# Performance work log

Hardware: AMD Instinct MI355X
Metric: run time of the kernel (lower is better)

Reference implementation:

```python
import jax, jax.numpy as jnp
import numpy as np

H, E, DFF = 1024, 8, 4096


def setup_inputs() -> dict:
    key = jax.random.key(0)
    ks = jax.random.split(key, 7)
    s = lambda *shape: 1.0 / np.sqrt(shape[-2] if len(shape) > 1 else shape[-1])
    x = jax.random.normal(ks[0], (2, 2048, H), dtype=jnp.float32)
    Wr = jax.random.normal(ks[1], (H, E), dtype=jnp.float32) * (1.0 / np.sqrt(H))
    br = jnp.zeros((E,), dtype=jnp.float32)
    W1 = jax.random.normal(ks[2], (E, H, DFF), dtype=jnp.float32) * (1.0 / np.sqrt(H))
    b1 = jnp.zeros((E, DFF), dtype=jnp.float32)
    W2 = jax.random.normal(ks[3], (E, DFF, H), dtype=jnp.float32) * (1.0 / np.sqrt(DFF))
    b2 = jnp.zeros((E, H), dtype=jnp.float32)
    return {"x": x, "Wr": Wr, "br": br, "W1": W1, "b1": b1, "W2": W2, "b2": b2}


def reference(x, Wr, br, W1, b1, W2, b2):
    B, S, Hd = x.shape
    n_exp = W1.shape[0]
    xt = x.reshape(-1, Hd)                      # (T, H)
    logits = xt @ Wr + br                       # (T, E)
    probs = jax.nn.softmax(logits, axis=-1)
    gate = jnp.max(probs, axis=-1)              # (T,) top-1 gate value
    idx = jnp.argmax(probs, axis=-1)            # (T,) chosen expert
    # dense all-expert FFN, then one-hot combine (vectorized equivalent of per-token loop)
    h1 = jnp.maximum(jnp.einsum('th,ehf->etf', xt, W1) + b1[:, None, :], 0.0)  # (E,T,DFF)
    ye = jnp.einsum('etf,efh->eth', h1, W2) + b2[:, None, :]                   # (E,T,H)
    onehot = jax.nn.one_hot(idx, n_exp, dtype=xt.dtype)                        # (T,E)
    y = jnp.einsum('te,eth->th', onehot, ye) * gate[:, None]                   # (T,H)
    return y.reshape(B, S, Hd)
```

## Files before the change

kernel.cpp:

```cpp
#include <hip/hip_runtime.h>
#include <stdint.h>

typedef unsigned short u16;
typedef __attribute__((ext_vector_type(8))) short s16x8;
typedef __attribute__((ext_vector_type(4))) float f32x4;
typedef __attribute__((ext_vector_type(4))) unsigned uint4v;

#define NEXP 8
#define HD 1024
#define DFF 4096
#define BM 128
#define BN 128
#define BK 64

#define CT_S 136
#define TILE_U16 (BM * BK)

__device__ __forceinline__ u16 f2bf(float f) {
  union { float f; unsigned u; } c; c.f = f;
  unsigned r = c.u + 0x7fffu + ((c.u >> 16) & 1u);
  return (u16)(r >> 16);
}

__device__ __forceinline__ unsigned cvtpk(float a, float b) {
  unsigned r;
  asm("v_cvt_pk_bf16_f32 %0, %1, %2" : "=v"(r) : "v"(a), "v"(b));
  return r;
}

__device__ __forceinline__ void gload_lds16(const void* g, const void* l) {
  __builtin_amdgcn_global_load_lds(
      (const __attribute__((address_space(1))) unsigned int*)(uintptr_t)g,
      (__attribute__((address_space(3))) unsigned int*)(unsigned)(uintptr_t)l,
      16, 0, 0);
}

__global__ __launch_bounds__(64) void zero_k(int* counts) {
  if (threadIdx.x < NEXP) counts[threadIdx.x] = 0;
}

template <int K, int N>
__device__ __forceinline__ void convt_tile(const float* __restrict__ W,
    u16* __restrict__ Wt, int idx, u16* __restrict__ T) {
  const int e = idx >> 9;
  const int ti = idx & 511;
  const int k0 = (ti % (K / 128)) * 128;
  const int n0 = (ti / (K / 128)) * 64;
  const float* src = W + (size_t)e * K * N;
  u16* dst = Wt + (size_t)e * K * N;
  const int t = threadIdx.x;
  const int m = t & 15, g = t >> 4;
  const int kq = g * 8, nq = m * 4;
  f32x4 v[8];
#pragma unroll
  for (int i = 0; i < 8; ++i)
    v[i] = *(const f32x4*)(src + (size_t)(k0 + kq + i) * N + n0 + nq);
#pragma unroll
  for (int j = 0; j < 4; ++j) {
    uint4v q;
    q[0] = cvtpk(v[0][j], v[1][j]);
    q[1] = cvtpk(v[2][j], v[3][j]);
    q[2] = cvtpk(v[4][j], v[5][j]);
    q[3] = cvtpk(v[6][j], v[7][j]);
    *(uint4v*)&T[(nq + j) * CT_S + kq] = q;
  }
  __syncthreads();
#pragma unroll
  for (int r = 0; r < 4; ++r) {
    const int nn = r * 16 + g;
    const int c8 = m * 8;
    uint4v q = *(const uint4v*)&T[nn * CT_S + c8];
    *(uint4v*)(dst + (size_t)(n0 + nn) * K + k0 + c8) = q;
  }
}

__global__ __launch_bounds__(256) void prep1_k(
    const float* __restrict__ x, const float* __restrict__ Wr,
    const float* __restrict__ br, int* __restrict__ counts,
    int* __restrict__ tok_exp, float* __restrict__ tok_gate,
    const float* __restrict__ W1, u16* __restrict__ W1t,
    u16* __restrict__ Xbf, int T) {
  __shared__ __align__(16) u16 Tt[64 * CT_S];
  const int bid = blockIdx.x;
  const int NBR = T / 4;
  if (bid >= NBR) {
    convt_tile<HD, DFF>(W1, W1t, bid - NBR, Tt);
    return;
  }
  const int w = threadIdx.x >> 6, l = threadIdx.x & 63;
  const int t = bid * 4 + w;
  const float4* xr = (const float4*)(x + (size_t)t * HD);
  float acc[NEXP];
#pragma unroll
  for (int j = 0; j < NEXP; ++j) acc[j] = 0.f;
#pragma unroll
  for (int i = 0; i < 4; ++i) {
    float4 v = xr[l + i * 64];
    unsigned pa = cvtpk(v.x, v.y), pb = cvtpk(v.z, v.w);
    *(uint2*)&Xbf[(size_t)t * HD + (l + i * 64) * 4] = make_uint2(pa, pb);
    const int h = (l + i * 64) * 4;
    const float* w0 = Wr + (size_t)h * NEXP;
#pragma unroll
    for (int c = 0; c < 4; ++c) {
      float xv = (c == 0) ? v.x : (c == 1) ? v.y : (c == 2) ? v.z : v.w;
      const float4* wr4 = (const float4*)(w0 + c * NEXP);
      float4 a = wr4[0], b = wr4[1];
      acc[0] += xv * a.x; acc[1] += xv * a.y; acc[2] += xv * a.z; acc[3] += xv * a.w;
      acc[4] += xv * b.x; acc[5] += xv * b.y; acc[6] += xv * b.z; acc[7] += xv * b.w;
    }
  }
#pragma unroll
  for (int j = 0; j < NEXP; ++j)
#pragma unroll
    for (int off = 32; off > 0; off >>= 1) acc[j] += __shfl_xor(acc[j], off);
  if (l == 0) {
    float lg[NEXP];
    float best = acc[0] + br[0]; int bi = 0;
    lg[0] = best;
#pragma unroll
    for (int j = 1; j < NEXP; ++j) {
      lg[j] = acc[j] + br[j];
      if (lg[j] > best) { best = lg[j]; bi = j; }
    }
    float s = 0.f;
#pragma unroll
    for (int j = 0; j < NEXP; ++j) s += expf(lg[j] - best);
    tok_exp[t] = bi;
    tok_gate[t] = 1.0f / s;
    atomicAdd(&counts[bi], 1);
  }
}

__global__ __launch_bounds__(64) void scan_k(const int* __restrict__ counts,
    int* __restrict__ seg, int* __restrict__ cursor,
    int* __restrict__ ntile, int* __restrict__ tile_e, int* __restrict__ tile_m) {
  if (threadIdx.x == 0) {
    int s = 0, nt = 0;
#pragma unroll
    for (int e = 0; e < NEXP; ++e) {
      seg[e] = s; cursor[e] = s;
      int c = counts[e];
      for (int m = 0; m < c; m += BM) { tile_e[nt] = e; tile_m[nt] = m; ++nt; }
      s += c;
    }
    seg[NEXP] = s;
    ntile[0] = nt;
  }
}

__global__ __launch_bounds__(256) void gather_k(const u16* __restrict__ Xbf,
    const int* __restrict__ tok_exp, const float* __restrict__ tok_gate,
    int* __restrict__ cursor, int* __restrict__ perm, float* __restrict__ gatep,
    u16* __restrict__ Xg) {
  const int w = threadIdx.x >> 6, l = threadIdx.x & 63;
  const int t = blockIdx.x * 4 + w;
  int pos = 0;
  if (l == 0) {
    int e = tok_exp[t];
    pos = atomicAdd(&cursor[e], 1);
    perm[pos] = t;
    gatep[pos] = tok_gate[t];
  }
  pos = __shfl(pos, 0);
  const s16x8* srcr = (const s16x8*)(Xbf + (size_t)t * HD);
  s16x8* dst = (s16x8*)(Xg + (size_t)pos * HD);
#pragma unroll
  for (int i = 0; i < HD / 8 / 64; ++i)
    dst[l + i * 64] = srcr[l + i * 64];
}

template <int KD, int ND, int EPI, int KSPLIT>
__device__ __forceinline__ void gemm_body(
    u16* __restrict__ sh,
    const u16* __restrict__ A, const u16* __restrict__ Bt,
    const float* __restrict__ bias, const int* __restrict__ seg,
    const int* __restrict__ ntile, const int* __restrict__ tile_e,
    const int* __restrict__ tile_m,
    u16* __restrict__ H1out, float* __restrict__ Pt,
    int bx, int by, int ks) {
  if (by >= ntile[0]) return;
  const int e  = tile_e[by];
  const int m0 = tile_m[by];
  const int s0 = seg[e];
  const int cnt = seg[e + 1] - s0;
  const int n0 = bx * BN;
  constexpr int NT = (KD / KSPLIT) / BK;
  const int kbase = ks * (KD / KSPLIT);

  const int t = threadIdx.x;
  const int l = t & 63, w = t >> 6;
  const int wr = w >> 1, wc = w & 1;

  const f32x4 fzero = {0.f, 0.f, 0.f, 0.f};
  f32x4 acc[4][4];
#pragma unroll
  for (int i = 0; i < 4; ++i)
#pragma unroll
    for (int j = 0; j < 4; ++j) acc[i][j] = fzero;

  const int sub = t & 7, r8 = t >> 3;
  const int koff = (sub ^ (r8 & 7)) * 8;
  int aoff[4], boff[4];
  const u16* bte = Bt + (size_t)e * ND * KD;
#pragma unroll
  for (int c = 0; c < 4; ++c) {
    int row = c * 32 + r8;
    int rg = m0 + row; if (rg >= cnt) rg = cnt - 1;
    aoff[c] = (s0 + rg) * KD + kbase + koff;
    boff[c] = (n0 + row) * KD + kbase + koff;
  }

  u16* Ac = sh;
  u16* Bc = sh + TILE_U16;
  u16* An = sh + 2 * TILE_U16;
  u16* Bn = sh + 3 * TILE_U16;

#define STAGE(pa, pb, tt) do { \
    const int ko_ = (tt) * BK; \
    _Pragma("unroll") for (int c_ = 0; c_ < 4; ++c_) \
      gload_lds16(A + (size_t)aoff[c_] + ko_, (pa) + (c_ * 256 + t) * 8); \
    _Pragma("unroll") for (int c_ = 0; c_ < 4; ++c_) \
      gload_lds16(bte + (size_t)boff[c_] + ko_, (pb) + (c_ * 256 + t) * 8); \
  } while (0)

#define COMPUTE(pa, pb) do { \
    _Pragma("unroll") for (int s_ = 0; s_ < 2; ++s_) { \
      const int fo_ = ((s_ * 4 + (l >> 4)) ^ (l & 7)) * 8; \
      s16x8 af_[4], bf_[4]; \
      _Pragma("unroll") for (int mi_ = 0; mi_ < 4; ++mi_) \
        af_[mi_] = *(const s16x8*)&(pa)[(wr * 64 + mi_ * 16 + (l & 15)) * BK + fo_]; \
      _Pragma("unroll") for (int ni_ = 0; ni_ < 4; ++ni_) \
        bf_[ni_] = *(const s16x8*)&(pb)[(wc * 64 + ni_ * 16 + (l & 15)) * BK + fo_]; \
      _Pragma("unroll") for (int mi_ = 0; mi_ < 4; ++mi_) \
        _Pragma("unroll") for (int ni_ = 0; ni_ < 4; ++ni_) \
          acc[mi_][ni_] = __builtin_amdgcn_mfma_f32_16x16x32_bf16(af_[mi_], bf_[ni_], acc[mi_][ni_], 0, 0, 0); \
    } \
  } while (0)

  STAGE(Ac, Bc, 0);
  __syncthreads();
  for (int tt = 0; tt < NT; ++tt) {
    if (tt + 1 < NT) STAGE(An, Bn, tt + 1);
    COMPUTE(Ac, Bc);
    if (tt + 1 < NT) {
      __syncthreads();
      u16* x;
      x = Ac; Ac = An; An = x;
      x = Bc; Bc = Bn; Bn = x;
    }
  }

#undef STAGE
#undef COMPUTE

  const int lr = (l >> 4) * 4;
  const int lc = l & 15;

  if constexpr (EPI == 0) {
    float bv2[4];
#pragma unroll
    for (int ni = 0; ni < 4; ++ni)
      bv2[ni] = bias[(size_t)e * ND + n0 + wc * 64 + ni * 16 + lc];
#pragma unroll
    for (int mi = 0; mi < 4; ++mi) {
#pragma unroll
      for (int r = 0; r < 4; ++r) {
        int row = m0 + wr * 64 + mi * 16 + lr + r;
        if (row < cnt) {
          u16* hrow = H1out + (size_t)(s0 + row) * ND + n0 + wc * 64;
#pragma unroll
          for (int ni = 0; ni < 4; ++ni) {
            float v = acc[mi][ni][r] + bv2[ni];
            v = v > 0.f ? v : 0.f;
            hrow[ni * 16 + lc] = f2bf(v);
          }
        }
      }
    }
  } else {
    const int totT = seg[NEXP];
#pragma unroll
    for (int mi = 0; mi < 4; ++mi) {
#pragma unroll
      for (int r = 0; r < 4; ++r) {
        int row = m0 + wr * 64 + mi * 16 + lr + r;
        if (row < cnt) {
          float* prow = Pt + ((size_t)ks * totT + s0 + row) * ND + n0 + wc * 64;
#pragma unroll
          for (int ni = 0; ni < 4; ++ni)
            prow[ni * 16 + lc] = acc[mi][ni][r];
        }
      }
    }
  }
}

__global__ __launch_bounds__(256, 2) void gemm1_fused_k(
    const u16* __restrict__ Xg, const u16* __restrict__ W1t,
    const float* __restrict__ b1, const int* __restrict__ seg,
    const int* __restrict__ ntile, const int* __restrict__ tile_e,
    const int* __restrict__ tile_m, u16* __restrict__ H1,
    const float* __restrict__ W2, u16* __restrict__ W2t, int ng1) {
  __shared__ __align__(16) u16 sh[4 * TILE_U16];
  const int bid = blockIdx.x;
  if (bid < ng1) {
    gemm_body<HD, DFF, 0, 1>(sh, Xg, W1t, b1, seg, ntile, tile_e,
                             tile_m, H1, nullptr, bid % (DFF / BN), bid / (DFF / BN), 0);
  } else {
    convt_tile<DFF, HD>(W2, W2t, bid - ng1, sh);
  }
}

__global__ __launch_bounds__(256, 2) void gemm2_k(
    const u16* __restrict__ H1, const u16* __restrict__ W2t,
    const int* __restrict__ seg, const int* __restrict__ ntile,
    const int* __restrict__ tile_e, const int* __restrict__ tile_m,
    float* __restrict__ Pt) {
  __shared__ __align__(16) u16 sh[4 * TILE_U16];
  gemm_body<DFF, HD, 2, 4>(sh, H1, W2t, nullptr, seg, ntile, tile_e,
                           tile_m, nullptr, Pt, blockIdx.x, blockIdx.y, blockIdx.z);
}

__global__ __launch_bounds__(256) void reduce_k(const float* __restrict__ Pt,
    const float* __restrict__ b2, const int* __restrict__ perm,
    const float* __restrict__ gatep, const int* __restrict__ tok_exp,
    float* __restrict__ out) {
  const int pos = blockIdx.x;
  const int totT = gridDim.x;
  const int tok = perm[pos];
  const float g = gatep[pos];
  const int e = tok_exp[tok];
  const int h = threadIdx.x * 4;
  float4 s = *(const float4*)(Pt + ((size_t)0 * totT + pos) * HD + h);
#pragma unroll
  for (int k = 1; k < 4; ++k) {
    float4 p = *(const float4*)(Pt + ((size_t)k * totT + pos) * HD + h);
    s.x += p.x; s.y += p.y; s.z += p.z; s.w += p.w;
  }
  float4 b = *(const float4*)(b2 + (size_t)e * HD + h);
  float4 o;
  o.x = (s.x + b.x) * g; o.y = (s.y + b.y) * g;
  o.z = (s.z + b.z) * g; o.w = (s.w + b.w) * g;
  *(float4*)(out + (size_t)tok * HD + h) = o;
}

extern "C" void kernel_launch(void* const* d_in, const int* in_sizes, int n_in,
                              void* d_out, int out_size, void* d_ws, size_t ws_size,
                              hipStream_t stream) {
  const float* x  = (const float*)d_in[0];
  const float* Wr = (const float*)d_in[1];
  const float* br = (const float*)d_in[2];
  const float* W1 = (const float*)d_in[3];
  const float* b1 = (const float*)d_in[4];
  const float* W2 = (const float*)d_in[5];
  const float* b2 = (const float*)d_in[6];
  float* out = (float*)d_out;

  const int T = in_sizes[0] / HD;
  char* ws = (char*)d_ws;
  int*   counts   = (int*)(ws + 0);
  int*   cursor   = (int*)(ws + 64);
  int*   seg      = (int*)(ws + 128);
  int*   ntile    = (int*)(ws + 192);
  int*   tile_e   = (int*)(ws + 256);
  int*   tile_m   = (int*)(ws + 512);
  int*   tok_exp  = (int*)(ws + 1024);
  float* tok_gate = (float*)(ws + 1024 + 4 * (size_t)T);
  int*   perm     = (int*)(ws + 1024 + 8 * (size_t)T);
  float* gatep    = (float*)(ws + 1024 + 12 * (size_t)T);
  u16*   Xg       = (u16*)(ws + 1024 + 16 * (size_t)T);
  u16*   H1       = (u16*)(ws + 1024 + 16 * (size_t)T + 2 * (size_t)T * HD);
  size_t off2     = 1024 + 16 * (size_t)T + 2 * (size_t)T * HD + 2 * (size_t)T * DFF;
  u16*   W1t      = (u16*)(ws + off2);
  u16*   W2t      = (u16*)(ws + off2 + 2 * (size_t)NEXP * HD * DFF);
  float* Pt       = (float*)W1t;
  u16*   Xbf      = H1;

  hipLaunchKernelGGL(zero_k, dim3(1), dim3(64), 0, stream, counts);
  const int NBR = T / 4;
  const int NCT = 512 * NEXP;
  hipLaunchKernelGGL(prep1_k, dim3(NBR + NCT), dim3(256), 0, stream,
                     x, Wr, br, counts, tok_exp, tok_gate, W1, W1t, Xbf, T);
  hipLaunchKernelGGL(scan_k, dim3(1), dim3(64), 0, stream, counts, seg, cursor, ntile, tile_e, tile_m);
  hipLaunchKernelGGL(gather_k, dim3(T / 4), dim3(256), 0, stream,
                     Xbf, tok_exp, tok_gate, cursor, perm, gatep, Xg);
  const int maxtile = (T + BM - 1) / BM + NEXP - 1;
  const int ng1 = (DFF / BN) * maxtile;
  hipLaunchKernelGGL(gemm1_fused_k, dim3(ng1 + NCT), dim3(256), 0, stream,
                     Xg, W1t, b1, seg, ntile, tile_e, tile_m, H1, W2, W2t, ng1);
  hipLaunchKernelGGL(gemm2_k, dim3(HD / BN, maxtile, 4), dim3(256), 0, stream,
                     H1, W2t, seg, ntile, tile_e, tile_m, Pt);
  hipLaunchKernelGGL(reduce_k, dim3(T), dim3(256), 0, stream, Pt, b2, perm, gatep, tok_exp, out);
}
```

Baseline: 298.7 us.

## Use direct-to-LDS loads for weight transpose and count experts in scan kernel

The fp32-to-bf16 weight transpose now stages raw fp32 tiles into LDS with global_load_lds, then each thread reads a column and writes 32 contiguous bf16 values, replacing the register-convert-then-LDS path. Expert counting moves from per-token atomics in the router kernel into the scan kernel, which histograms tok_exp with a wavefront reduction, so the zero kernel launch goes away. The new LDS read pattern (stride 64 floats per row) may cause bank conflicts, and the single-wave scan now reads all T tokens serially.

```diff
diff --git a/kernel.cpp b/kernel.cpp
--- a/kernel.cpp
+++ b/kernel.cpp
@@ -13,7 +13,6 @@
 #define BN 128
 #define BK 64
 
-#define CT_S 136
 #define TILE_U16 (BM * BK)
 
 __device__ __forceinline__ u16 f2bf(float f) {
@@ -35,56 +34,52 @@
       16, 0, 0);
 }
 
-__global__ __launch_bounds__(64) void zero_k(int* counts) {
-  if (threadIdx.x < NEXP) counts[threadIdx.x] = 0;
-}
-
 template <int K, int N>
-__device__ __forceinline__ void convt_tile(const float* __restrict__ W,
-    u16* __restrict__ Wt, int idx, u16* __restrict__ T) {
+__device__ __forceinline__ void convt_gl(const float* __restrict__ W,
+    u16* __restrict__ Wt, int idx, float* __restrict__ Tf) {
   const int e = idx >> 9;
   const int ti = idx & 511;
   const int k0 = (ti % (K / 128)) * 128;
   const int n0 = (ti / (K / 128)) * 64;
-  const float* src = W + (size_t)e * K * N;
-  u16* dst = Wt + (size_t)e * K * N;
   const int t = threadIdx.x;
-  const int m = t & 15, g = t >> 4;
-  const int kq = g * 8, nq = m * 4;
-  f32x4 v[8];
-#pragma unroll
-  for (int i = 0; i < 8; ++i)
-    v[i] = *(const f32x4*)(src + (size_t)(k0 + kq + i) * N + n0 + nq);
-#pragma unroll
-  for (int j = 0; j < 4; ++j) {
-    uint4v q;
-    q[0] = cvtpk(v[0][j], v[1][j]);
-    q[1] = cvtpk(v[2][j], v[3][j]);
-    q[2] = cvtpk(v[4][j], v[5][j]);
-    q[3] = cvtpk(v[6][j], v[7][j]);
-    *(uint4v*)&T[(nq + j) * CT_S + kq] = q;
+  const float* src = W + (size_t)e * K * N + (size_t)k0 * N + n0;
+#pragma unroll
+  for (int c = 0; c < 8; ++c) {
+    int slot = c * 256 + t;
+    gload_lds16(src + (size_t)(slot >> 4) * N + (slot & 15) * 4, Tf + slot * 4);
   }
   __syncthreads();
-#pragma unroll
-  for (int r = 0; r < 4; ++r) {
-    const int nn = r * 16 + g;
-    const int c8 = m * 8;
-    uint4v q = *(const uint4v*)&T[nn * CT_S + c8];
-    *(uint4v*)(dst + (size_t)(n0 + nn) * K + k0 + c8) = q;
-  }
+  const int n = t >> 2, ks = t & 3;
+  float v[32];
+#pragma unroll
+  for (int j = 0; j < 32; ++j)
+    v[j] = Tf[(ks * 32 + j) * 64 + n];
+  uint4v q0, q1, q2, q3;
+#pragma unroll
+  for (int a = 0; a < 4; ++a) {
+    q0[a] = cvtpk(v[2 * a], v[2 * a + 1]);
+    q1[a] = cvtpk(v[8 + 2 * a], v[9 + 2 * a]);
+    q2[a] = cvtpk(v[16 + 2 * a], v[17 + 2 * a]);
+    q3[a] = cvtpk(v[24 + 2 * a], v[25 + 2 * a]);
+  }
+  u16* d = Wt + (size_t)e * K * N + (size_t)(n0 + n) * K + k0 + ks * 32;
+  *(uint4v*)d = q0;
+  *(uint4v*)(d + 8) = q1;
+  *(uint4v*)(d + 16) = q2;
+  *(uint4v*)(d + 24) = q3;
 }
 
 __global__ __launch_bounds__(256) void prep1_k(
     const float* __restrict__ x, const float* __restrict__ Wr,
-    const float* __restrict__ br, int* __restrict__ counts,
+    const float* __restrict__ br,
     int* __restrict__ tok_exp, float* __restrict__ tok_gate,
     const float* __restrict__ W1, u16* __restrict__ W1t,
     u16* __restrict__ Xbf, int T) {
-  __shared__ __align__(16) u16 Tt[64 * CT_S];
+  __shared__ __align__(16) float Tf[128 * 64];
   const int bid = blockIdx.x;
   const int NBR = T / 4;
   if (bid >= NBR) {
-    convt_tile<HD, DFF>(W1, W1t, bid - NBR, Tt);
+    convt_gl<HD, DFF>(W1, W1t, bid - NBR, Tf);
     return;
   }
   const int w = threadIdx.x >> 6, l = threadIdx.x & 63;
@@ -127,19 +122,31 @@
     for (int j = 0; j < NEXP; ++j) s += expf(lg[j] - best);
     tok_exp[t] = bi;
     tok_gate[t] = 1.0f / s;
-    atomicAdd(&counts[bi], 1);
-  }
-}
-
-__global__ __launch_bounds__(64) void scan_k(const int* __restrict__ counts,
+  }
+}
+
+__global__ __launch_bounds__(64) void scan_k(const int* __restrict__ tok_exp, int T,
     int* __restrict__ seg, int* __restrict__ cursor,
     int* __restrict__ ntile, int* __restrict__ tile_e, int* __restrict__ tile_m) {
-  if (threadIdx.x == 0) {
+  const int l = threadIdx.x;
+  int cnt[NEXP];
+#pragma unroll
+  for (int j = 0; j < NEXP; ++j) cnt[j] = 0;
+  for (int i = l; i < T; i += 64) {
+    int e = tok_exp[i];
+#pragma unroll
+    for (int j = 0; j < NEXP; ++j) cnt[j] += (e == j) ? 1 : 0;
+  }
+#pragma unroll
+  for (int j = 0; j < NEXP; ++j)
+#pragma unroll
+    for (int off = 32; off > 0; off >>= 1) cnt[j] += __shfl_xor(cnt[j], off);
+  if (l == 0) {
     int s = 0, nt = 0;
 #pragma unroll
     for (int e = 0; e < NEXP; ++e) {
       seg[e] = s; cursor[e] = s;
-      int c = counts[e];
+      int c = cnt[e];
       for (int m = 0; m < c; m += BM) { tile_e[nt] = e; tile_m[nt] = m; ++nt; }
       s += c;
     }
@@ -244,9 +251,9 @@
     COMPUTE(Ac, Bc);
     if (tt + 1 < NT) {
       __syncthreads();
-      u16* x;
-      x = Ac; Ac = An; An = x;
-      x = Bc; Bc = Bn; Bn = x;
+      u16* xp;
+      xp = Ac; Ac = An; An = xp;
+      xp = Bc; Bc = Bn; Bn = xp;
     }
   }
 
@@ -307,7 +314,7 @@
     gemm_body<HD, DFF, 0, 1>(sh, Xg, W1t, b1, seg, ntile, tile_e,
                              tile_m, H1, nullptr, bid % (DFF / BN), bid / (DFF / BN), 0);
   } else {
-    convt_tile<DFF, HD>(W2, W2t, bid - ng1, sh);
+    convt_gl<DFF, HD>(W2, W2t, bid - ng1, (float*)sh);
   }
 }
 
@@ -358,7 +365,6 @@
 
   const int T = in_sizes[0] / HD;
   char* ws = (char*)d_ws;
-  int*   counts   = (int*)(ws + 0);
   int*   cursor   = (int*)(ws + 64);
   int*   seg      = (int*)(ws + 128);
   int*   ntile    = (int*)(ws + 192);
@@ -376,12 +382,12 @@
   float* Pt       = (float*)W1t;
   u16*   Xbf      = H1;
 
-  hipLaunchKernelGGL(zero_k, dim3(1), dim3(64), 0, stream, counts);
   const int NBR = T / 4;
   const int NCT = 512 * NEXP;
   hipLaunchKernelGGL(prep1_k, dim3(NBR + NCT), dim3(256), 0, stream,
-                     x, Wr, br, counts, tok_exp, tok_gate, W1, W1t, Xbf, T);
-  hipLaunchKernelGGL(scan_k, dim3(1), dim3(64), 0, stream, counts, seg, cursor, ntile, tile_e, tile_m);
+                     x, Wr, br, tok_exp, tok_gate, W1, W1t, Xbf, T);
+  hipLaunchKernelGGL(scan_k, dim3(1), dim3(64), 0, stream,
+                     tok_exp, T, seg, cursor, ntile, tile_e, tile_m);
   hipLaunchKernelGGL(gather_k, dim3(T / 4), dim3(256), 0, stream,
                      Xbf, tok_exp, tok_gate, cursor, perm, gatep, Xg);
   const int maxtile = (T + BM - 1) / BM + NEXP - 1;
```

After: 290.2 us. 2.9% less time.
